# Kernel optimization log

Hardware: AMD Instinct MI355X
Metric: run time of the kernel (lower is better)

Reference implementation:

```python
import jax, jax.numpy as jnp
import numpy as np

N_NODES = 50000
N_EDGES = 800000
D_IN = 788
D_HID = 256
N_REL = 7
N_CLS = 2


def rgcn_conv(x, w_rel, w_root, b, src, dst, edge_type):
    """PyG RGCNConv with default mean aggregation per relation + root weight + bias.
    x: (N, F_in); w_rel: (R, F_in, F_out); w_root: (F_in, F_out); b: (F_out,).
    src/dst: (E,) with edge_index[0]=source j, edge_index[1]=target i.
    """
    R, _, F_out = w_rel.shape
    N = x.shape[0]
    # transform-then-gather (equivalent to PyG's gather-then-transform, cheaper)
    x_rel = jnp.einsum('nf,rfo->rno', x, w_rel)          # (R, N, F_out)
    msg = x_rel[edge_type, src]                           # (E, F_out)
    agg = jnp.zeros((R, N, F_out), x.dtype).at[edge_type, dst].add(msg)
    cnt = jnp.zeros((R, N), x.dtype).at[edge_type, dst].add(1.0)
    out = (agg / jnp.clip(cnt, 1.0)[..., None]).sum(0)    # mean per relation, summed over relations
    return out + x @ w_root + b


def setup_inputs() -> dict:
    key = jax.random.key(0)
    ks = jax.random.split(key, 9)
    x = jax.random.normal(ks[0], (N_NODES, D_IN), dtype=jnp.float32)
    edge_index = jax.random.randint(ks[1], (2, N_EDGES), 0, N_NODES, dtype=jnp.int64)
    edge_type = jax.random.randint(ks[2], (N_EDGES,), 0, N_REL, dtype=jnp.int64)
    s1 = 0.05
    w1_rel = jax.random.normal(ks[3], (N_REL, D_IN, D_HID), dtype=jnp.float32) * s1
    w1_root = jax.random.normal(ks[4], (D_IN, D_HID), dtype=jnp.float32) * s1
    b1 = jnp.zeros((D_HID,), dtype=jnp.float32)
    w2_rel = jax.random.normal(ks[5], (N_REL, D_HID, N_CLS), dtype=jnp.float32) * s1
    w2_root = jax.random.normal(ks[6], (D_HID, N_CLS), dtype=jnp.float32) * s1
    b2 = jnp.zeros((N_CLS,), dtype=jnp.float32)
    return {"x": x, "edge_index": edge_index, "edge_type": edge_type,
            "w1_rel": w1_rel, "w1_root": w1_root, "b1": b1,
            "w2_rel": w2_rel, "w2_root": w2_root, "b2": b2}


def reference(x, edge_index, edge_type, w1_rel, w1_root, b1, w2_rel, w2_root, b2):
    src, dst = edge_index[0], edge_index[1]
    h = jax.nn.relu(rgcn_conv(x, w1_rel, w1_root, b1, src, dst, edge_type))
    # F.dropout(p=0.5) is identity in eval mode
    out = rgcn_conv(h, w2_rel, w2_root, b2, src, dst, edge_type)
    return out
```

## Files before the change

### kernel.cpp

```cpp
#include <hip/hip_runtime.h>
#include <hip/hip_bf16.h>
#include <stdint.h>

#define N_NODES 50000
#define N_EDGES 800000
#define D_IN    788
#define D_INP   800
#define D_HID   256
#define N_REL   7
#define NBINS   (N_REL * N_NODES)
#define NSCANB  342
#define NXTILE  391

typedef __attribute__((ext_vector_type(8))) short bf16x8;
typedef __attribute__((ext_vector_type(4))) float f32x4;
typedef __attribute__((ext_vector_type(4))) unsigned int u32x4;

__device__ __forceinline__ unsigned short f2bf(float f) {
  union { __hip_bfloat16 h; unsigned short u; } v;
  v.h = __float2bfloat16(f);
  return v.u;
}

__device__ __forceinline__ f32x4 bf4(ushort4 g) {
  union { unsigned int u; float f; } a, b, c, d;
  a.u = (unsigned)g.x << 16; b.u = (unsigned)g.y << 16;
  c.u = (unsigned)g.z << 16; d.u = (unsigned)g.w << 16;
  return (f32x4){a.f, b.f, c.f, d.f};
}

#define GLOAD16(g, l) __builtin_amdgcn_global_load_lds(                      \
    (const __attribute__((address_space(1))) unsigned int*)(g),              \
    (__attribute__((address_space(3))) unsigned int*)(l), 16, 0, 0)

__global__ void k_conv_w(const float* __restrict__ w_rel, const float* __restrict__ w_root,
                         unsigned short* __restrict__ wt) {
  int b = blockIdx.x;
  int m = b / 25, chunk = b % 25;
  int o = threadIdx.x;
  const float* src = (m < N_REL) ? (w_rel + (size_t)m * D_IN * D_HID) : w_root;
  int k0 = chunk * 32;

  unsigned short v[32];
#pragma unroll
  for (int kk = 0; kk < 32; kk++) {
    int k = k0 + kk;
    v[kk] = (k < D_IN) ? f2bf(src[(size_t)k * D_HID + o]) : (unsigned short)0;
  }

  unsigned short* dst = wt + ((size_t)m * D_HID + o) * D_INP + chunk * 32;
  int sw = (o >> 1) & 3;
#pragma unroll
  for (int g = 0; g < 4; g++) {
    union { unsigned short us[8]; u32x4 u; } pk;
#pragma unroll
    for (int j = 0; j < 8; j++) pk.us[j] = v[g * 8 + j];
    *(u32x4*)(dst + (g ^ sw) * 8) = pk.u;
  }
}

__global__ void k_xbf(const float* __restrict__ x, unsigned short* __restrict__ xb) {
  int t = blockIdx.x * blockDim.x + threadIdx.x;
  if (t >= N_NODES * 100) return;
  int n = t / 100, gi = t % 100;
  int chunk = gi >> 2, p = gi & 3;
  int g = p ^ ((n >> 1) & 3);
  int c = chunk * 32 + g * 8;
  union { unsigned short us[8]; u32x4 v; } pk;
  if (c + 7 < D_IN) {
    float4 a = *(const float4*)(x + (size_t)n * D_IN + c);
    float4 b = *(const float4*)(x + (size_t)n * D_IN + c + 4);
    pk.us[0] = f2bf(a.x); pk.us[1] = f2bf(a.y); pk.us[2] = f2bf(a.z); pk.us[3] = f2bf(a.w);
    pk.us[4] = f2bf(b.x); pk.us[5] = f2bf(b.y); pk.us[6] = f2bf(b.z); pk.us[7] = f2bf(b.w);
  } else {
#pragma unroll
    for (int j = 0; j < 8; j++)
      pk.us[j] = (c + j < D_IN) ? f2bf(x[(size_t)n * D_IN + c + j]) : (unsigned short)0;
  }
  *(u32x4*)(xb + (size_t)n * D_INP + chunk * 32 + p * 8) = pk.v;
}

__global__ void k_count(const int* __restrict__ etype, const int* __restrict__ edst,
                        int* __restrict__ cnt) {
  int t = blockIdx.x * blockDim.x + threadIdx.x;
  if (t >= N_EDGES) return;
  atomicAdd(&cnt[etype[t] * N_NODES + edst[t]], 1);
}

__global__ void k_scan1(const int* __restrict__ cnt, int* __restrict__ bsum) {
  __shared__ int wsh[4];
  int b = blockIdx.x, tid = threadIdx.x;
  int base = b * 1024 + tid * 4;
  int4 v = {0, 0, 0, 0};
  if (base + 3 < NBINS) v = *(const int4*)(cnt + base);
  else { for (int i = 0; i < 4; i++) if (base + i < NBINS) ((int*)&v)[i] = cnt[base + i]; }
  int s = v.x + v.y + v.z + v.w;
  for (int o = 32; o > 0; o >>= 1) s += __shfl_down(s, o);
  if ((tid & 63) == 0) wsh[tid >> 6] = s;
  __syncthreads();
  if (tid == 0) bsum[b] = wsh[0] + wsh[1] + wsh[2] + wsh[3];
}

__global__ void k_scan2(const int* __restrict__ bsum, int* __restrict__ boff) {
  __shared__ int tmp[512];
  int tid = threadIdx.x;
  int mine = (tid < NSCANB) ? bsum[tid] : 0;
  tmp[tid] = mine;
  __syncthreads();
  for (int o = 1; o < 512; o <<= 1) {
    int v = (tid >= o) ? tmp[tid - o] : 0;
    __syncthreads();
    tmp[tid] += v;
    __syncthreads();
  }
  if (tid < NSCANB) boff[tid] = tmp[tid] - mine;
}

__global__ void k_scan3(const int* __restrict__ cnt, const int* __restrict__ boff,
                        int* __restrict__ S) {
  __shared__ int wsum[4];
  int b = blockIdx.x, tid = threadIdx.x;
  int base = b * 1024 + tid * 4;
  int4 v = {0, 0, 0, 0};
  if (base + 3 < NBINS) v = *(const int4*)(cnt + base);
  else { for (int i = 0; i < 4; i++) if (base + i < NBINS) ((int*)&v)[i] = cnt[base + i]; }
  int s = v.x + v.y + v.z + v.w;
  int lane = tid & 63, w = tid >> 6;
  int sc = s;
  for (int o = 1; o < 64; o <<= 1) { int u = __shfl_up(sc, o); if (lane >= o) sc += u; }
  if (lane == 63) wsum[w] = sc;
  __syncthreads();
  int wbase = 0;
  for (int i = 0; i < w; i++) wbase += wsum[i];
  int excl = boff[b] + wbase + sc - s;
  int o0 = excl, o1 = excl + v.x, o2 = o1 + v.y, o3 = o2 + v.z;
  if (base + 3 < NBINS) { int4 o4 = {o0, o1, o2, o3}; *(int4*)(S + base) = o4; }
  else {
    if (base     < NBINS) S[base]     = o0;
    if (base + 1 < NBINS) S[base + 1] = o1;
    if (base + 2 < NBINS) S[base + 2] = o2;
    if (base + 3 < NBINS) S[base + 3] = o3;
  }
}

__global__ void k_scatter(const int* __restrict__ etype, const int* __restrict__ edst,
                          const int* __restrict__ esrc, const int* __restrict__ S,
                          int* __restrict__ rank, int* __restrict__ psrc) {
  int t = blockIdx.x * blockDim.x + threadIdx.x;
  if (t >= N_EDGES) return;
  int bin = etype[t] * N_NODES + edst[t];
  int r = atomicAdd(&rank[bin], 1);
  psrc[S[bin] + r] = esrc[t];
}

template<int SWZ, int NMAT>
__global__ __launch_bounds__(512) void k_gemm_g(
    const unsigned short* __restrict__ xb, const unsigned short* __restrict__ wt,
    unsigned short* __restrict__ xrs, int mb) {
  __shared__ __align__(16) unsigned short As[2][128 * 32];
  __shared__ __align__(16) unsigned short Bs[2][256 * 32];

  int tid = threadIdx.x;
  int bx, by;
  if (SWZ) {
    int b = blockIdx.x;
    int l = (b % 8) * (NXTILE * NMAT / 8) + b / 8;
    bx = l / NMAT; by = l % NMAT;
  } else {
    bx = blockIdx.x; by = blockIdx.y;
  }
  int mat = mb + by;
  int m0 = bx * 128;
  const unsigned short* wsec = wt + (size_t)mat * (D_HID * D_INP);
  int lane = tid & 63, w = tid >> 6;
  int wm = w >> 2, wn = w & 3;

  int ar = tid >> 2;
  int arow = m0 + ar; if (arow > N_NODES - 1) arow = N_NODES - 1;
  const unsigned short* asrc = xb + (size_t)arow * D_INP + (tid & 3) * 8;
  const unsigned short* bsrc0 = wsec + (size_t)(tid >> 2) * D_INP + (tid & 3) * 8;
  const unsigned short* bsrc1 = bsrc0 + (size_t)128 * D_INP;

  f32x4 acc[4][4];
#pragma unroll
  for (int i = 0; i < 4; i++)
#pragma unroll
    for (int j = 0; j < 4; j++) acc[i][j] = (f32x4){0.f, 0.f, 0.f, 0.f};

  int row = lane & 15, quad = lane >> 4;
  int rg = (quad ^ ((row >> 1) & 3)) * 8;

  GLOAD16(asrc,  &As[0][0] + tid * 8);
  GLOAD16(bsrc0, &Bs[0][0] + tid * 8);
  GLOAD16(bsrc1, &Bs[0][0] + 4096 + tid * 8);
  __syncthreads();

  int cur = 0;
  for (int ks = 0; ks < 25; ks++) {
    if (ks < 24) {
      int ko = (ks + 1) * 32;
      GLOAD16(asrc + ko,  &As[cur ^ 1][0] + tid * 8);
      GLOAD16(bsrc0 + ko, &Bs[cur ^ 1][0] + tid * 8);
      GLOAD16(bsrc1 + ko, &Bs[cur ^ 1][0] + 4096 + tid * 8);
    }

    const unsigned short* Ac = &As[cur][0];
    const unsigned short* Bc = &Bs[cur][0];
    bf16x8 af[4], bfr[4];
#pragma unroll
    for (int i = 0; i < 4; i++)
      af[i] = *(const bf16x8*)(Ac + (wm * 64 + i * 16 + row) * 32 + rg);
#pragma unroll
    for (int j = 0; j < 4; j++)
      bfr[j] = *(const bf16x8*)(Bc + (wn * 64 + j * 16 + row) * 32 + rg);
#pragma unroll
    for (int i = 0; i < 4; i++)
#pragma unroll
      for (int j = 0; j < 4; j++)
        acc[i][j] = __builtin_amdgcn_mfma_f32_16x16x32_bf16(af[i], bfr[j], acc[i][j], 0, 0, 0);

    __syncthreads();
    cur ^= 1;
  }

  int col_l = lane & 15, rquad = lane >> 4;
  unsigned short* xo = xrs + (size_t)by * ((size_t)N_NODES * D_HID);
#pragma unroll
  for (int i = 0; i < 4; i++) {
#pragma unroll
    for (int reg = 0; reg < 4; reg++) {
      int node = m0 + wm * 64 + i * 16 + rquad * 4 + reg;
      if (node < N_NODES) {
#pragma unroll
        for (int j = 0; j < 4; j++)
          xo[(size_t)node * D_HID + wn * 64 + j * 16 + col_l] = f2bf(acc[i][j][reg]);
      }
    }
  }
}

__global__ __launch_bounds__(256) void k_gemm_f(
    const float* __restrict__ x, const unsigned short* __restrict__ wt,
    unsigned short* __restrict__ xrs, int mb) {
  __shared__ __align__(16) unsigned short As[64 * 40];
  __shared__ __align__(16) unsigned short Bs[256 * 40];

  int tid = threadIdx.x;
  int mat = mb + blockIdx.y;
  int m0 = blockIdx.x * 64;
  const unsigned short* wsec = wt + (size_t)mat * (D_HID * D_INP);
  int lane = tid & 63, w = tid >> 6;

  int ra = tid >> 2, ca = tid & 3, ca8 = ca * 8;
  int arow = m0 + ra; if (arow > N_NODES - 1) arow = N_NODES - 1;
  const float* apf = x + (size_t)arow * D_IN;
  const unsigned short* bgp = wsec + (size_t)ra * D_INP + (ca ^ ((ra >> 1) & 3)) * 8;
  unsigned short* al = As + ra * 40 + ca8;
  unsigned short* bl = Bs + ra * 40 + ca8;

  f32x4 acc[4][4];
#pragma unroll
  for (int i = 0; i < 4; i++)
#pragma unroll
    for (int j = 0; j < 4; j++) acc[i][j] = (f32x4){0.f, 0.f, 0.f, 0.f};

  float4 pa0 = *(const float4*)(apf + ca8);
  float4 pa1 = *(const float4*)(apf + ca8 + 4);
  u32x4 pb0 = *(const u32x4*)(bgp);
  u32x4 pb1 = *(const u32x4*)(bgp +  64 * D_INP);
  u32x4 pb2 = *(const u32x4*)(bgp + 128 * D_INP);
  u32x4 pb3 = *(const u32x4*)(bgp + 192 * D_INP);

  int row = lane & 15, quad = lane >> 4;
  for (int ks = 0; ks < 25; ks++) {
    if (ks < 24) {
      union { unsigned short us[8]; u32x4 v; } pk;
      pk.us[0] = f2bf(pa0.x); pk.us[1] = f2bf(pa0.y);
      pk.us[2] = f2bf(pa0.z); pk.us[3] = f2bf(pa0.w);
      pk.us[4] = f2bf(pa1.x); pk.us[5] = f2bf(pa1.y);
      pk.us[6] = f2bf(pa1.z); pk.us[7] = f2bf(pa1.w);
      *(u32x4*)al = pk.v;
    } else {
      float v0 = pa0.x, v1 = pa0.y, v2 = pa0.z, v3 = pa0.w;
      float v4 = pa1.x, v5 = pa1.y, v6 = pa1.z, v7 = pa1.w;
      if (ca8 == 16) { v0 = pa1.x; v1 = pa1.y; v2 = pa1.z; v3 = pa1.w;
                       v4 = 0.f; v5 = 0.f; v6 = 0.f; v7 = 0.f; }
      if (ca8 == 24) { v0 = 0.f; v1 = 0.f; v2 = 0.f; v3 = 0.f;
                       v4 = 0.f; v5 = 0.f; v6 = 0.f; v7 = 0.f; }
      union { unsigned short us[8]; u32x4 v; } pk;
      pk.us[0] = f2bf(v0); pk.us[1] = f2bf(v1); pk.us[2] = f2bf(v2); pk.us[3] = f2bf(v3);
      pk.us[4] = f2bf(v4); pk.us[5] = f2bf(v5); pk.us[6] = f2bf(v6); pk.us[7] = f2bf(v7);
      *(u32x4*)al = pk.v;
    }
    *(u32x4*)bl = pb0;
    *(u32x4*)(bl +  64 * 40) = pb1;
    *(u32x4*)(bl + 128 * 40) = pb2;
    *(u32x4*)(bl + 192 * 40) = pb3;
    __syncthreads();

    if (ks < 24) {
      int on = (ks + 1) * 32 + ca8;
      int lo = (on > 780) ? 780 : on;
      pa0 = *(const float4*)(apf + lo);
      pa1 = *(const float4*)(apf + lo + 4);
      int ko = (ks + 1) * 32;
      pb0 = *(const u32x4*)(bgp + ko);
      pb1 = *(const u32x4*)(bgp + ko +  64 * D_INP);
      pb2 = *(const u32x4*)(bgp + ko + 128 * D_INP);
      pb3 = *(const u32x4*)(bgp + ko + 192 * D_INP);
    }

    bf16x8 af[4], bfr[4];
#pragma unroll
    for (int i = 0; i < 4; i++)
      af[i] = *(const bf16x8*)(As + (i * 16 + row) * 40 + quad * 8);
#pragma unroll
    for (int j = 0; j < 4; j++)
      bfr[j] = *(const bf16x8*)(Bs + (w * 64 + j * 16 + row) * 40 + quad * 8);
#pragma unroll
    for (int i = 0; i < 4; i++)
#pragma unroll
      for (int j = 0; j < 4; j++)
        acc[i][j] = __builtin_amdgcn_mfma_f32_16x16x32_bf16(af[i], bfr[j], acc[i][j], 0, 0, 0);
    __syncthreads();
  }

  int col_l = lane & 15, rquad = lane >> 4;
  unsigned short* xo = xrs + (size_t)blockIdx.y * ((size_t)N_NODES * D_HID);
#pragma unroll
  for (int i = 0; i < 4; i++) {
#pragma unroll
    for (int reg = 0; reg < 4; reg++) {
      int node = m0 + i * 16 + rquad * 4 + reg;
      if (node < N_NODES) {
#pragma unroll
        for (int j = 0; j < 4; j++)
          xo[(size_t)node * D_HID + w * 64 + j * 16 + col_l] = f2bf(acc[i][j][reg]);
      }
    }
  }
}

__global__ __launch_bounds__(256) void k_agg8(
    const unsigned short* __restrict__ xrs, const int* __restrict__ S,
    const int* __restrict__ cnt, const int* __restrict__ psrc,
    const float* __restrict__ b1, const float* __restrict__ w2rel,
    const float* __restrict__ w2root, float* __restrict__ y) {
  __shared__ float hsh[4][256];
  int wv = threadIdx.x >> 6;
  int n = blockIdx.x * 4 + wv;
  int lane = threadIdx.x & 63;
  if (n >= N_NODES) return;

  int c_l = 0, p_l = 0;
  if (lane < N_REL) {
    c_l = cnt[lane * N_NODES + n];
    p_l = S[lane * N_NODES + n];
  }

  f32x4 acc = (f32x4){0.f, 0.f, 0.f, 0.f};
#pragma unroll
  for (int r = 0; r < N_REL; r++) {
    int c = __shfl(c_l, r);
    if (c > 0) {
      int p = __shfl(p_l, r);
      const unsigned short* slab = xrs + (size_t)r * N_NODES * D_HID;
      f32x4 s = (f32x4){0.f, 0.f, 0.f, 0.f};
      int e = 0;
      for (; e + 1 < c; e += 2) {
        int s0 = psrc[p + e], s1 = psrc[p + e + 1];
        ushort4 g0 = *(const ushort4*)(slab + (size_t)s0 * D_HID + lane * 4);
        ushort4 g1 = *(const ushort4*)(slab + (size_t)s1 * D_HID + lane * 4);
        s += bf4(g0) + bf4(g1);
      }
      if (e < c) {
        int s0 = psrc[p + e];
        ushort4 g0 = *(const ushort4*)(slab + (size_t)s0 * D_HID + lane * 4);
        s += bf4(g0);
      }
      acc += s * (1.0f / (float)c);
    }
  }

  ushort4 gr = *(const ushort4*)(xrs + ((size_t)7 * N_NODES + n) * D_HID + lane * 4);
  acc += bf4(gr);
  f32x4 b = *(const f32x4*)(b1 + lane * 4);
  f32x4 hv;
  hv[0] = fmaxf(acc[0] + b[0], 0.f);
  hv[1] = fmaxf(acc[1] + b[1], 0.f);
  hv[2] = fmaxf(acc[2] + b[2], 0.f);
  hv[3] = fmaxf(acc[3] + b[3], 0.f);

  *(f32x4*)&hsh[wv][lane * 4] = hv;
  __builtin_amdgcn_wave_barrier();

  int m = lane >> 3, sl = lane & 7;
  const float* wp = (m < N_REL) ? (w2rel + m * (D_HID * 2)) : w2root;
  float d0 = 0.f, d1 = 0.f;
#pragma unroll
  for (int j = 0; j < 8; j++) {
    int db = sl * 4 + j * 32;
    f32x4 h4 = *(const f32x4*)&hsh[wv][db];
    f32x4 wa = *(const f32x4*)(wp + db * 2);
    f32x4 wb = *(const f32x4*)(wp + db * 2 + 4);
    d0 += h4[0] * wa[0] + h4[1] * wa[2] + h4[2] * wb[0] + h4[3] * wb[2];
    d1 += h4[0] * wa[1] + h4[1] * wa[3] + h4[2] * wb[1] + h4[3] * wb[3];
  }
  d0 += __shfl_down(d0, 1); d1 += __shfl_down(d1, 1);
  d0 += __shfl_down(d0, 2); d1 += __shfl_down(d1, 2);
  d0 += __shfl_down(d0, 4); d1 += __shfl_down(d1, 4);
  if (sl == 0) {
    y[(size_t)m * (N_NODES * 2) + n * 2]     = d0;
    y[(size_t)m * (N_NODES * 2) + n * 2 + 1] = d1;
  }
}

__global__ __launch_bounds__(256) void k_agg(
    const unsigned short* __restrict__ xrs, const int* __restrict__ S,
    const int* __restrict__ cnt, const int* __restrict__ psrc,
    float* __restrict__ h, const float* __restrict__ b1,
    const float* __restrict__ w2rel, const float* __restrict__ w2root,
    float* __restrict__ y, int r0, int pass) {
  int n = blockIdx.x * 4 + (threadIdx.x >> 6);
  int lane = threadIdx.x & 63;
  if (n >= N_NODES) return;
  f32x4 acc;
  if (pass == 0) acc = (f32x4){0.f, 0.f, 0.f, 0.f};
  else acc = *(const f32x4*)(h + (size_t)n * D_HID + lane * 4);

  int nr = (pass < 3) ? 2 : 1;
  for (int rr = 0; rr < nr; rr++) {
    int bin = (r0 + rr) * N_NODES + n;
    int c = cnt[bin];
    if (c > 0) {
      int p = S[bin];
      f32x4 s = (f32x4){0.f, 0.f, 0.f, 0.f};
      int e = 0;
      for (; e + 1 < c; e += 2) {
        int s0 = psrc[p + e], s1 = psrc[p + e + 1];
        ushort4 g0 = *(const ushort4*)(xrs + ((size_t)rr * N_NODES + s0) * D_HID + lane * 4);
        ushort4 g1 = *(const ushort4*)(xrs + ((size_t)rr * N_NODES + s1) * D_HID + lane * 4);
        s += bf4(g0) + bf4(g1);
      }
      if (e < c) {
        int s0 = psrc[p + e];
        ushort4 g0 = *(const ushort4*)(xrs + ((size_t)rr * N_NODES + s0) * D_HID + lane * 4);
        s += bf4(g0);
      }
      acc += s * (1.0f / (float)c);
    }
  }

  if (pass < 3) {
    *(f32x4*)(h + (size_t)n * D_HID + lane * 4) = acc;
    return;
  }

  ushort4 gr = *(const ushort4*)(xrs + ((size_t)1 * N_NODES + n) * D_HID + lane * 4);
  acc += bf4(gr);
  f32x4 b = *(const f32x4*)(b1 + lane * 4);
  f32x4 hv;
  hv[0] = fmaxf(acc[0] + b[0], 0.f);
  hv[1] = fmaxf(acc[1] + b[1], 0.f);
  hv[2] = fmaxf(acc[2] + b[2], 0.f);
  hv[3] = fmaxf(acc[3] + b[3], 0.f);

#pragma unroll
  for (int m = 0; m < 8; m++) {
    const float* wp = (m < N_REL) ? (w2rel + m * (D_HID * 2)) : w2root;
    f32x4 wa = *(const f32x4*)(wp + lane * 8);
    f32x4 wb = *(const f32x4*)(wp + lane * 8 + 4);
    float d0 = hv[0] * wa[0] + hv[1] * wa[2] + hv[2] * wb[0] + hv[3] * wb[2];
    float d1 = hv[0] * wa[1] + hv[1] * wa[3] + hv[2] * wb[1] + hv[3] * wb[3];
#pragma unroll
    for (int off = 32; off > 0; off >>= 1) {
      d0 += __shfl_down(d0, off);
      d1 += __shfl_down(d1, off);
    }
    if (lane == 0) {
      y[(size_t)m * (N_NODES * 2) + n * 2]     = d0;
      y[(size_t)m * (N_NODES * 2) + n * 2 + 1] = d1;
    }
  }
}

__global__ void k_out(const float* __restrict__ y, const float* __restrict__ b2,
                      const int* __restrict__ cnt, const int* __restrict__ S,
                      const int* __restrict__ psrc, float* __restrict__ out) {
  int t = blockIdx.x * blockDim.x + threadIdx.x;
  if (t < NBINS) {
    int c = cnt[t];
    if (c == 0) return;
    int p = S[t];
    int r = t / N_NODES;
    int i = t - r * N_NODES;
    const float* yr = y + (size_t)r * (N_NODES * 2);
    float s0 = 0.f, s1 = 0.f;
    for (int e = 0; e < c; e++) {
      int sc = psrc[p + e];
      float2 v = *(const float2*)(yr + sc * 2);
      s0 += v.x; s1 += v.y;
    }
    float is = 1.0f / (float)c;
    atomicAdd(out + (size_t)i * 2,     s0 * is);
    atomicAdd(out + (size_t)i * 2 + 1, s1 * is);
  } else if (t < NBINS + N_NODES) {
    int i = t - NBINS;
    float2 v = *(const float2*)(y + (size_t)N_REL * (N_NODES * 2) + i * 2);
    atomicAdd(out + (size_t)i * 2,     v.x + b2[0]);
    atomicAdd(out + (size_t)i * 2 + 1, v.y + b2[1]);
  }
}

#define OFF_WT   0u
#define OFF_XRS  3276800u
#define OFF_H    54476800u
#define OFF_CNT  105676800u
#define OFF_RANK 107076800u
#define OFF_S    108476800u
#define OFF_PSRC 109876800u
#define OFF_Y    113076800u
#define OFF_BSUM 116276800u
#define OFF_BOFF 116278848u
#define OFF_XB   116280896u
#define WS_NEED_XB 196280896ull

#define F_OFF_WT   0u
#define F_OFF_XRS  3276800u
#define F_OFF_CNT  208076800u
#define F_OFF_RANK 209476800u
#define F_OFF_S    210876800u
#define F_OFF_PSRC 212276800u
#define F_OFF_Y    215476800u
#define F_OFF_BSUM 218676800u
#define F_OFF_BOFF 218678848u
#define F_OFF_XB   218680896u
#define WS_NEED_FULL 298680896ull

extern "C" void kernel_launch(void* const* d_in, const int* in_sizes, int n_in,
                              void* d_out, int out_size, void* d_ws, size_t ws_size,
                              hipStream_t stream) {
  const float* x      = (const float*)d_in[0];
  const int*   eidx   = (const int*)d_in[1];
  const int*   etype  = (const int*)d_in[2];
  const float* w1rel  = (const float*)d_in[3];
  const float* w1root = (const float*)d_in[4];
  const float* b1     = (const float*)d_in[5];
  const float* w2rel  = (const float*)d_in[6];
  const float* w2root = (const float*)d_in[7];
  const float* b2     = (const float*)d_in[8];
  float* out = (float*)d_out;
  char* ws = (char*)d_ws;
  const int* esrc = eidx;
  const int* edst = eidx + N_EDGES;

  const bool full = (ws_size >= WS_NEED_FULL);
  const bool big  = !full && (ws_size >= WS_NEED_XB);

  hipMemsetAsync(d_out, 0, (size_t)out_size * sizeof(float), stream);

  if (full) {
    unsigned short* wt  = (unsigned short*)(ws + F_OFF_WT);
    unsigned short* xrs = (unsigned short*)(ws + F_OFF_XRS);
    int*   cnt  = (int*)(ws + F_OFF_CNT);
    int*   rank = (int*)(ws + F_OFF_RANK);
    int*   S    = (int*)(ws + F_OFF_S);
    int*   psrc = (int*)(ws + F_OFF_PSRC);
    float* y    = (float*)(ws + F_OFF_Y);
    int*   bsum = (int*)(ws + F_OFF_BSUM);
    int*   boff = (int*)(ws + F_OFF_BOFF);
    unsigned short* xb = (unsigned short*)(ws + F_OFF_XB);

    hipMemsetAsync(ws + F_OFF_CNT, 0, 2800000u, stream);

    k_conv_w<<<8 * 25, 256, 0, stream>>>(w1rel, w1root, wt);
    k_xbf<<<(N_NODES * 100 + 255) / 256, 256, 0, stream>>>(x, xb);
    k_count<<<(N_EDGES + 255) / 256, 256, 0, stream>>>(etype, edst, cnt);
    k_scan1<<<NSCANB, 256, 0, stream>>>(cnt, bsum);
    k_scan2<<<1, 512, 0, stream>>>(bsum, boff);
    k_scan3<<<NSCANB, 256, 0, stream>>>(cnt, boff, S);
    k_scatter<<<(N_EDGES + 255) / 256, 256, 0, stream>>>(etype, edst, esrc, S, rank, psrc);

    k_gemm_g<1, 8><<<NXTILE * 8, 512, 0, stream>>>(xb, wt, xrs, 0);
    k_agg8<<<(N_NODES + 3) / 4, 256, 0, stream>>>(xrs, S, cnt, psrc,
                                                  b1, w2rel, w2root, y);
    k_out<<<(NBINS + N_NODES + 255) / 256, 256, 0, stream>>>(y, b2, cnt, S, psrc, out);
    return;
  }

  unsigned short* wt  = (unsigned short*)(ws + OFF_WT);
  unsigned short* xrs = (unsigned short*)(ws + OFF_XRS);
  float* h    = (float*)(ws + OFF_H);
  int*   cnt  = (int*)(ws + OFF_CNT);
  int*   rank = (int*)(ws + OFF_RANK);
  int*   S    = (int*)(ws + OFF_S);
  int*   psrc = (int*)(ws + OFF_PSRC);
  float* y    = (float*)(ws + OFF_Y);
  int*   bsum = (int*)(ws + OFF_BSUM);
  int*   boff = (int*)(ws + OFF_BOFF);
  unsigned short* xb = (unsigned short*)(ws + OFF_XB);

  hipMemsetAsync(ws + OFF_CNT, 0, 2800000u, stream);

  k_conv_w<<<8 * 25, 256, 0, stream>>>(w1rel, w1root, wt);
  if (big)
    k_xbf<<<(N_NODES * 100 + 255) / 256, 256, 0, stream>>>(x, xb);
  k_count<<<(N_EDGES + 255) / 256, 256, 0, stream>>>(etype, edst, cnt);
  k_scan1<<<NSCANB, 256, 0, stream>>>(cnt, bsum);
  k_scan2<<<1, 512, 0, stream>>>(bsum, boff);
  k_scan3<<<NSCANB, 256, 0, stream>>>(cnt, boff, S);
  k_scatter<<<(N_EDGES + 255) / 256, 256, 0, stream>>>(etype, edst, esrc, S, rank, psrc);

  for (int p = 0; p < 4; p++) {
    if (big)
      k_gemm_g<0, 2><<<dim3(NXTILE, 2), 512, 0, stream>>>(xb, wt, xrs, 2 * p);
    else
      k_gemm_f<<<dim3(782, 2), 256, 0, stream>>>(x, wt, xrs, 2 * p);
    k_agg<<<(N_NODES + 3) / 4, 256, 0, stream>>>(xrs, S, cnt, psrc, h,
                                                 b1, w2rel, w2root, y, 2 * p, p);
  }

  k_out<<<(NBINS + N_NODES + 255) / 256, 256, 0, stream>>>(y, b2, cnt, S, psrc, out);
}
```

Measured before the change: 711.9 us.

## Use 64-wide K tiles with chunk-pair swizzle in bf16 GEMM, pad K to 832

Pads the reduction dimension from 800 to 832 and changes the packed layouts of x and the weights so that 32-wide K chunks are swapped in pairs by row parity. The main GEMM now loads 64-wide K tiles in 13 steps instead of 32-wide tiles in 25, and the swizzle lets adjacent rows read different halves to cut LDS bank conflicts. It drops the LDS double buffering: loads and compute now alternate with a sync after each load. The aim is fewer sync and loop iterations per tile, at the cost of exposed load latency, extra padded work, and larger workspace offsets.

```diff
diff --git a/kernel.cpp b/kernel.cpp
--- a/kernel.cpp
+++ b/kernel.cpp
@@ -5,7 +5,7 @@
 #define N_NODES 50000
 #define N_EDGES 800000
 #define D_IN    788
-#define D_INP   800
+#define D_INP   832
 #define D_HID   256
 #define N_REL   7
 #define NBINS   (N_REL * N_NODES)
@@ -33,13 +33,15 @@
     (const __attribute__((address_space(1))) unsigned int*)(g),              \
     (__attribute__((address_space(3))) unsigned int*)(l), 16, 0, 0)
 
+
 __global__ void k_conv_w(const float* __restrict__ w_rel, const float* __restrict__ w_root,
                          unsigned short* __restrict__ wt) {
   int b = blockIdx.x;
-  int m = b / 25, chunk = b % 25;
+  int m = b / 26, pc = b % 26;
   int o = threadIdx.x;
   const float* src = (m < N_REL) ? (w_rel + (size_t)m * D_IN * D_HID) : w_root;
-  int k0 = chunk * 32;
+  int cc = pc ^ (o & 1);
+  int k0 = cc * 32;
 
   unsigned short v[32];
 #pragma unroll
@@ -48,7 +50,7 @@
     v[kk] = (k < D_IN) ? f2bf(src[(size_t)k * D_HID + o]) : (unsigned short)0;
   }
 
-  unsigned short* dst = wt + ((size_t)m * D_HID + o) * D_INP + chunk * 32;
+  unsigned short* dst = wt + ((size_t)m * D_HID + o) * D_INP + pc * 32;
   int sw = (o >> 1) & 3;
 #pragma unroll
   for (int g = 0; g < 4; g++) {
@@ -61,11 +63,12 @@
 
 __global__ void k_xbf(const float* __restrict__ x, unsigned short* __restrict__ xb) {
   int t = blockIdx.x * blockDim.x + threadIdx.x;
-  if (t >= N_NODES * 100) return;
-  int n = t / 100, gi = t % 100;
-  int chunk = gi >> 2, p = gi & 3;
+  if (t >= N_NODES * 104) return;
+  int n = t / 104, gi = t % 104;
+  int pc = gi >> 2, p = gi & 3;
+  int cc = pc ^ (n & 1);
   int g = p ^ ((n >> 1) & 3);
-  int c = chunk * 32 + g * 8;
+  int c = cc * 32 + g * 8;
   union { unsigned short us[8]; u32x4 v; } pk;
   if (c + 7 < D_IN) {
     float4 a = *(const float4*)(x + (size_t)n * D_IN + c);
@@ -77,7 +80,7 @@
     for (int j = 0; j < 8; j++)
       pk.us[j] = (c + j < D_IN) ? f2bf(x[(size_t)n * D_IN + c + j]) : (unsigned short)0;
   }
-  *(u32x4*)(xb + (size_t)n * D_INP + chunk * 32 + p * 8) = pk.v;
+  *(u32x4*)(xb + (size_t)n * D_INP + pc * 32 + p * 8) = pk.v;
 }
 
 __global__ void k_count(const int* __restrict__ etype, const int* __restrict__ edst,
@@ -157,8 +160,8 @@
 __global__ __launch_bounds__(512) void k_gemm_g(
     const unsigned short* __restrict__ xb, const unsigned short* __restrict__ wt,
     unsigned short* __restrict__ xrs, int mb) {
-  __shared__ __align__(16) unsigned short As[2][128 * 32];
-  __shared__ __align__(16) unsigned short Bs[2][256 * 32];
+  __shared__ __align__(16) unsigned short As[128 * 64];
+  __shared__ __align__(16) unsigned short Bs[256 * 64];
 
   int tid = threadIdx.x;
   int bx, by;
@@ -175,11 +178,21 @@
   int lane = tid & 63, w = tid >> 6;
   int wm = w >> 2, wn = w & 3;
 
-  int ar = tid >> 2;
-  int arow = m0 + ar; if (arow > N_NODES - 1) arow = N_NODES - 1;
-  const unsigned short* asrc = xb + (size_t)arow * D_INP + (tid & 3) * 8;
-  const unsigned short* bsrc0 = wsec + (size_t)(tid >> 2) * D_INP + (tid & 3) * 8;
-  const unsigned short* bsrc1 = bsrc0 + (size_t)128 * D_INP;
+  int sr = tid >> 3, sg = (tid & 7) * 8;
+  int ar0 = m0 + sr;      if (ar0 > N_NODES - 1) ar0 = N_NODES - 1;
+  int ar1 = m0 + 64 + sr; if (ar1 > N_NODES - 1) ar1 = N_NODES - 1;
+  const unsigned short* asrc0 = xb + (size_t)ar0 * D_INP + sg;
+  const unsigned short* asrc1 = xb + (size_t)ar1 * D_INP + sg;
+  const unsigned short* bsrc0 = wsec + (size_t)sr * D_INP + sg;
+  const unsigned short* bsrc1 = bsrc0 + (size_t)64 * D_INP;
+  const unsigned short* bsrc2 = bsrc0 + (size_t)128 * D_INP;
+  const unsigned short* bsrc3 = bsrc0 + (size_t)192 * D_INP;
+  unsigned short* al0 = As + tid * 8;
+  unsigned short* al1 = As + 4096 + tid * 8;
+  unsigned short* bl0 = Bs + tid * 8;
+  unsigned short* bl1 = Bs + 4096 + tid * 8;
+  unsigned short* bl2 = Bs + 8192 + tid * 8;
+  unsigned short* bl3 = Bs + 12288 + tid * 8;
 
   f32x4 acc[4][4];
 #pragma unroll
@@ -189,38 +202,43 @@
 
   int row = lane & 15, quad = lane >> 4;
   int rg = (quad ^ ((row >> 1) & 3)) * 8;
-
-  GLOAD16(asrc,  &As[0][0] + tid * 8);
-  GLOAD16(bsrc0, &Bs[0][0] + tid * 8);
-  GLOAD16(bsrc1, &Bs[0][0] + 4096 + tid * 8);
-  __syncthreads();
-
-  int cur = 0;
-  for (int ks = 0; ks < 25; ks++) {
-    if (ks < 24) {
-      int ko = (ks + 1) * 32;
-      GLOAD16(asrc + ko,  &As[cur ^ 1][0] + tid * 8);
-      GLOAD16(bsrc0 + ko, &Bs[cur ^ 1][0] + tid * 8);
-      GLOAD16(bsrc1 + ko, &Bs[cur ^ 1][0] + 4096 + tid * 8);
-    }
-
-    const unsigned short* Ac = &As[cur][0];
-    const unsigned short* Bc = &Bs[cur][0];
+  int cp0 = (row & 1) * 32;
+  int cp1 = 32 - cp0;
+
+  for (int ks = 0; ks < 13; ks++) {
+    int ko = ks * 64;
+    GLOAD16(asrc0 + ko, al0);
+    GLOAD16(asrc1 + ko, al1);
+    GLOAD16(bsrc0 + ko, bl0);
+    GLOAD16(bsrc1 + ko, bl1);
+    GLOAD16(bsrc2 + ko, bl2);
+    GLOAD16(bsrc3 + ko, bl3);
+    __syncthreads();
+
     bf16x8 af[4], bfr[4];
 #pragma unroll
     for (int i = 0; i < 4; i++)
-      af[i] = *(const bf16x8*)(Ac + (wm * 64 + i * 16 + row) * 32 + rg);
+      af[i] = *(const bf16x8*)(As + (wm * 64 + i * 16 + row) * 64 + cp0 + rg);
 #pragma unroll
     for (int j = 0; j < 4; j++)
-      bfr[j] = *(const bf16x8*)(Bc + (wn * 64 + j * 16 + row) * 32 + rg);
+      bfr[j] = *(const bf16x8*)(Bs + (wn * 64 + j * 16 + row) * 64 + cp0 + rg);
 #pragma unroll
     for (int i = 0; i < 4; i++)
 #pragma unroll
       for (int j = 0; j < 4; j++)
         acc[i][j] = __builtin_amdgcn_mfma_f32_16x16x32_bf16(af[i], bfr[j], acc[i][j], 0, 0, 0);
-
+#pragma unroll
+    for (int i = 0; i < 4; i++)
+      af[i] = *(const bf16x8*)(As + (wm * 64 + i * 16 + row) * 64 + cp1 + rg);
+#pragma unroll
+    for (int j = 0; j < 4; j++)
+      bfr[j] = *(const bf16x8*)(Bs + (wn * 64 + j * 16 + row) * 64 + cp1 + rg);
+#pragma unroll
+    for (int i = 0; i < 4; i++)
+#pragma unroll
+      for (int j = 0; j < 4; j++)
+        acc[i][j] = __builtin_amdgcn_mfma_f32_16x16x32_bf16(af[i], bfr[j], acc[i][j], 0, 0, 0);
     __syncthreads();
-    cur ^= 1;
   }
 
   int col_l = lane & 15, rquad = lane >> 4;
@@ -252,6 +270,7 @@
   int lane = tid & 63, w = tid >> 6;
 
   int ra = tid >> 2, ca = tid & 3, ca8 = ca * 8;
+  int ra1 = ra & 1;
   int arow = m0 + ra; if (arow > N_NODES - 1) arow = N_NODES - 1;
   const float* apf = x + (size_t)arow * D_IN;
   const unsigned short* bgp = wsec + (size_t)ra * D_INP + (ca ^ ((ra >> 1) & 3)) * 8;
@@ -266,10 +285,11 @@
 
   float4 pa0 = *(const float4*)(apf + ca8);
   float4 pa1 = *(const float4*)(apf + ca8 + 4);
-  u32x4 pb0 = *(const u32x4*)(bgp);
-  u32x4 pb1 = *(const u32x4*)(bgp +  64 * D_INP);
-  u32x4 pb2 = *(const u32x4*)(bgp + 128 * D_INP);
-  u32x4 pb3 = *(const u32x4*)(bgp + 192 * D_INP);
+  int kb0 = ra1 * 32;
+  u32x4 pb0 = *(const u32x4*)(bgp + kb0);
+  u32x4 pb1 = *(const u32x4*)(bgp + kb0 +  64 * D_INP);
+  u32x4 pb2 = *(const u32x4*)(bgp + kb0 + 128 * D_INP);
+  u32x4 pb3 = *(const u32x4*)(bgp + kb0 + 192 * D_INP);
 
   int row = lane & 15, quad = lane >> 4;
   for (int ks = 0; ks < 25; ks++) {
@@ -303,7 +323,7 @@
       int lo = (on > 780) ? 780 : on;
       pa0 = *(const float4*)(apf + lo);
       pa1 = *(const float4*)(apf + lo + 4);
-      int ko = (ks + 1) * 32;
+      int ko = ((ks + 1) ^ ra1) * 32;
       pb0 = *(const u32x4*)(bgp + ko);
       pb1 = *(const u32x4*)(bgp + ko +  64 * D_INP);
       pb2 = *(const u32x4*)(bgp + ko + 128 * D_INP);
@@ -513,29 +533,29 @@
 }
 
 #define OFF_WT   0u
-#define OFF_XRS  3276800u
-#define OFF_H    54476800u
-#define OFF_CNT  105676800u
-#define OFF_RANK 107076800u
-#define OFF_S    108476800u
-#define OFF_PSRC 109876800u
-#define OFF_Y    113076800u
-#define OFF_BSUM 116276800u
-#define OFF_BOFF 116278848u
-#define OFF_XB   116280896u
-#define WS_NEED_XB 196280896ull
+#define OFF_XRS  3407872u
+#define OFF_H    54607872u
+#define OFF_CNT  105807872u
+#define OFF_RANK 107207872u
+#define OFF_S    108607872u
+#define OFF_PSRC 110007872u
+#define OFF_Y    113207872u
+#define OFF_BSUM 116407872u
+#define OFF_BOFF 116409920u
+#define OFF_XB   116411968u
+#define WS_NEED_XB 199611968ull
 
 #define F_OFF_WT   0u
-#define F_OFF_XRS  3276800u
-#define F_OFF_CNT  208076800u
-#define F_OFF_RANK 209476800u
-#define F_OFF_S    210876800u
-#define F_OFF_PSRC 212276800u
-#define F_OFF_Y    215476800u
-#define F_OFF_BSUM 218676800u
-#define F_OFF_BOFF 218678848u
-#define F_OFF_XB   218680896u
-#define WS_NEED_FULL 298680896ull
+#define F_OFF_XRS  3407872u
+#define F_OFF_CNT  208207872u
+#define F_OFF_RANK 209607872u
+#define F_OFF_S    211007872u
+#define F_OFF_PSRC 212407872u
+#define F_OFF_Y    215607872u
+#define F_OFF_BSUM 218807872u
+#define F_OFF_BOFF 218809920u
+#define F_OFF_XB   218811968u
+#define WS_NEED_FULL 302011968ull
 
 extern "C" void kernel_launch(void* const* d_in, const int* in_sizes, int n_in,
                               void* d_out, int out_size, void* d_ws, size_t ws_size,
@@ -573,8 +593,8 @@
 
     hipMemsetAsync(ws + F_OFF_CNT, 0, 2800000u, stream);
 
-    k_conv_w<<<8 * 25, 256, 0, stream>>>(w1rel, w1root, wt);
-    k_xbf<<<(N_NODES * 100 + 255) / 256, 256, 0, stream>>>(x, xb);
+    k_conv_w<<<8 * 26, 256, 0, stream>>>(w1rel, w1root, wt);
+    k_xbf<<<(N_NODES * 104 + 255) / 256, 256, 0, stream>>>(x, xb);
     k_count<<<(N_EDGES + 255) / 256, 256, 0, stream>>>(etype, edst, cnt);
     k_scan1<<<NSCANB, 256, 0, stream>>>(cnt, bsum);
     k_scan2<<<1, 512, 0, stream>>>(bsum, boff);
@@ -602,9 +622,9 @@
 
   hipMemsetAsync(ws + OFF_CNT, 0, 2800000u, stream);
 
-  k_conv_w<<<8 * 25, 256, 0, stream>>>(w1rel, w1root, wt);
+  k_conv_w<<<8 * 26, 256, 0, stream>>>(w1rel, w1root, wt);
   if (big)
-    k_xbf<<<(N_NODES * 100 + 255) / 256, 256, 0, stream>>>(x, xb);
+    k_xbf<<<(N_NODES * 104 + 255) / 256, 256, 0, stream>>>(x, xb);
   k_count<<<(N_EDGES + 255) / 256, 256, 0, stream>>>(etype, edst, cnt);
   k_scan1<<<NSCANB, 256, 0, stream>>>(cnt, bsum);
   k_scan2<<<1, 512, 0, stream>>>(bsum, boff);
```

Result: faster. 682.8 us (-4.1%).
